# Kernel optimization log

Measured on AMD Instinct MI355X. Metric: run time of the kernel, lower is better.

Reference implementation:

```python
import jax, jax.numpy as jnp
import numpy as np

LN_EPS = 1e-5
SUM_CLAMP = 1e-12


def setup_inputs() -> dict:
    key = jax.random.key(0)
    ks = jax.random.split(key, 10)
    L, D, H, P, E = 200000, 512, 512, 16384, 200000
    lesion_x = jax.random.normal(ks[0], (L, D), dtype=jnp.float32)
    edge_index = jnp.stack([
        jax.random.randint(ks[1], (E,), 0, P),   # patient idx
        jax.random.randint(ks[2], (E,), 0, L),   # lesion idx
    ], axis=0).astype(jnp.int64)
    s1 = 1.0 / np.sqrt(D)
    s2 = 1.0 / np.sqrt(H)
    W1 = jax.random.uniform(ks[3], (H, D), jnp.float32, -s1, s1)
    b1 = jax.random.uniform(ks[4], (H,), jnp.float32, -s1, s1)
    W2 = jax.random.uniform(ks[5], (1, H), jnp.float32, -s2, s2)
    b2 = jax.random.uniform(ks[6], (1,), jnp.float32, -s2, s2)
    Wp = jax.random.uniform(ks[7], (768, D), jnp.float32, -s1, s1)
    bp = jax.random.uniform(ks[8], (768,), jnp.float32, -s1, s1)
    gamma = jnp.ones((768,), jnp.float32)
    beta = jnp.zeros((768,), jnp.float32)
    return dict(lesion_x=lesion_x, patient_to_lesion_edge_index=edge_index,
                num_patients_in_batch=P, W1=W1, b1=b1, W2=W2, b2=b2,
                Wp=Wp, bp=bp, gamma=gamma, beta=beta)


def reference(lesion_x, patient_to_lesion_edge_index, num_patients_in_batch,
              W1, b1, W2, b2, Wp, bp, gamma, beta):
    P = int(num_patients_in_batch)
    pat = patient_to_lesion_edge_index[0]
    les = patient_to_lesion_edge_index[1]
    feats = lesion_x[les]                                  # [E, D] gather
    h = jnp.tanh(feats @ W1.T + b1)                        # [E, H]
    scores = (h @ W2.T + b2)[:, 0]                         # [E]
    smax = jax.ops.segment_max(scores, pat, num_segments=P)  # [P]
    ex = jnp.exp(scores - smax[pat])                       # [E]
    esum = jax.ops.segment_sum(ex, pat, num_segments=P)
    esum = jnp.maximum(esum, SUM_CLAMP)
    alpha = ex / esum[pat]                                 # [E]
    agg = jax.ops.segment_sum(feats * alpha[:, None], pat, num_segments=P)  # [P, D]
    proj = agg @ Wp.T + bp                                 # [P, 768]
    mu = jnp.mean(proj, axis=-1, keepdims=True)
    var = jnp.mean(jnp.square(proj - mu), axis=-1, keepdims=True)
    out = (proj - mu) * jax.lax.rsqrt(var + LN_EPS) * gamma + beta
    return out
```

## Files before the change

### kernel.cpp

```cpp
#include <hip/hip_runtime.h>
#include <hip/hip_bf16.h>

#define D_DIM 512
#define H_DIM 512
#define O_DIM 768

using bf16x8 = __attribute__((ext_vector_type(8))) short;
using f32x4  = __attribute__((ext_vector_type(4))) float;

static __device__ __forceinline__ unsigned cvtpk(float lo, float hi){
  unsigned r;
  asm("v_cvt_pk_bf16_f32 %0, %1, %2" : "=v"(r) : "v"(lo), "v"(hi));
  return r;
}

static __device__ __forceinline__ float bflo(unsigned u){
  return __uint_as_float(u << 16);
}
static __device__ __forceinline__ float bfhi(unsigned u){
  return __uint_as_float(u & 0xffff0000u);
}

static __device__ __forceinline__ float fast_tanh(float x){
  float e = __expf(2.f * x);
  return 1.f - 2.f / (e + 1.f);
}

static __device__ __forceinline__ unsigned f2ord(float f){
  unsigned u = __float_as_uint(f);
  return (u & 0x80000000u) ? ~u : (u | 0x80000000u);
}
static __device__ __forceinline__ float ord2f(unsigned u){
  u = (u & 0x80000000u) ? (u & 0x7fffffffu) : ~u;
  return __uint_as_float(u);
}

static __device__ __forceinline__ void gload16(const void* g, void* l){
  __builtin_amdgcn_global_load_lds(
      (const __attribute__((address_space(1))) void*)g,
      (__attribute__((address_space(3))) void*)l, 16, 0, 0);
}

__global__ void cvt_bf16(const float* __restrict__ in,
                         unsigned short* __restrict__ out, int n8)
{
  int stride = gridDim.x * blockDim.x;
  for (int i = blockIdx.x*blockDim.x + threadIdx.x; i < n8; i += stride){
    const float4* p = (const float4*)in + (size_t)i*2;
    float4 a = p[0], b = p[1];
    uint4 pk;
    pk.x = cvtpk(a.x, a.y);
    pk.y = cvtpk(a.z, a.w);
    pk.z = cvtpk(b.x, b.y);
    pk.w = cvtpk(b.z, b.w);
    ((uint4*)out)[i] = pk;
  }
}

__launch_bounds__(256, 2)
__global__ void gemm1_db(const float* __restrict__ A,
                         const short* __restrict__ Bm,
                         const float* __restrict__ bias,
                         const float* __restrict__ w2,
                         float* __restrict__ out,
                         short* __restrict__ Ab,
                         int M, int nwg)
{
  __shared__ short lds_a[2][128*64];
  __shared__ short lds_b[2][128*64];

  const int q  = nwg >> 3, rr = nwg & 7;
  const int xcd = blockIdx.x & 7, bidx = blockIdx.x >> 3;
  const int swz = (xcd < rr ? xcd*(q+1) : rr*(q+1) + (xcd-rr)*q) + bidx;
  const int colBase = (swz & 3) * 128;
  const int rowBase = (swz >> 2) * 128;
  const bool writeAb = (colBase == 0);

  const int tid  = threadIdx.x;
  const int lane = tid & 63;
  const int w    = tid >> 6;
  const int wr   = w >> 1, wc = w & 1;
  const int lr   = lane & 15;
  const int lk   = lane >> 4;

  const int srow = tid >> 4;
  const int sgf  = tid & 15;
  const int rlocB = lane >> 3;
  const int jB    = lane & 7;

  f32x4 acc[4][4];
  #pragma unroll
  for (int i = 0; i < 4; ++i)
    #pragma unroll
    for (int j = 0; j < 4; ++j)
      acc[i][j] = (f32x4){0.f, 0.f, 0.f, 0.f};

  float4 va[8];

  #pragma unroll
  for (int c = 0; c < 8; ++c){
    int gA = rowBase + c*16 + srow; if (gA > M-1) gA = M-1;
    va[c] = *(const float4*)(A + (size_t)gA*512 + sgf*4);
  }
  #pragma unroll
  for (int c = 0; c < 4; ++c){
    int rt = w*32 + c*8 + rlocB;
    int js = jB ^ (rt & 7);
    gload16(Bm + (size_t)(colBase + rt)*512 + js*8, &lds_b[0][(w*32 + c*8)*64]);
  }
  #pragma unroll
  for (int c = 0; c < 8; ++c){
    int rt = c*16 + srow;
    uint2 pk = { cvtpk(va[c].x, va[c].y), cvtpk(va[c].z, va[c].w) };
    int sidx = (rt*64 + sgf*4) ^ ((rt & 7) << 3);
    *(uint2*)&lds_a[0][sidx] = pk;
    if (writeAb){
      int gA = rowBase + rt;
      if (gA < M) *(uint2*)(Ab + (size_t)gA*512 + sgf*4) = pk;
    }
  }
  __syncthreads();

  int cur = 0;
  for (int kt = 0; kt < 8; ++kt){
    const int nxt = cur ^ 1;
    const int kNext = (kt + 1) * 64;
    if (kt < 7){
      #pragma unroll
      for (int c = 0; c < 8; ++c){
        int gA = rowBase + c*16 + srow; if (gA > M-1) gA = M-1;
        va[c] = *(const float4*)(A + (size_t)gA*512 + kNext + sgf*4);
      }
      #pragma unroll
      for (int c = 0; c < 4; ++c){
        int rt = w*32 + c*8 + rlocB;
        int js = jB ^ (rt & 7);
        gload16(Bm + (size_t)(colBase + rt)*512 + kNext + js*8,
                &lds_b[nxt][(w*32 + c*8)*64]);
      }
    }
    #pragma unroll
    for (int kk = 0; kk < 2; ++kk){
      bf16x8 af[4], bfr[4];
      #pragma unroll
      for (int mf = 0; mf < 4; ++mf){
        int r   = wr*64 + mf*16 + lr;
        int idx = (r*64 + kk*32 + lk*8) ^ ((r & 7) << 3);
        af[mf] = *(bf16x8*)&lds_a[cur][idx];
      }
      #pragma unroll
      for (int nf = 0; nf < 4; ++nf){
        int r   = wc*64 + nf*16 + lr;
        int idx = (r*64 + kk*32 + lk*8) ^ ((r & 7) << 3);
        bfr[nf] = *(bf16x8*)&lds_b[cur][idx];
      }
      __builtin_amdgcn_s_setprio(1);
      #pragma unroll
      for (int mf = 0; mf < 4; ++mf)
        #pragma unroll
        for (int nf = 0; nf < 4; ++nf)
          acc[mf][nf] = __builtin_amdgcn_mfma_f32_16x16x32_bf16(
              af[mf], bfr[nf], acc[mf][nf], 0, 0, 0);
      __builtin_amdgcn_s_setprio(0);
    }
    if (kt < 7){
      #pragma unroll
      for (int c = 0; c < 8; ++c){
        int rt = c*16 + srow;
        uint2 pk = { cvtpk(va[c].x, va[c].y), cvtpk(va[c].z, va[c].w) };
        int sidx = (rt*64 + sgf*4) ^ ((rt & 7) << 3);
        *(uint2*)&lds_a[nxt][sidx] = pk;
        if (writeAb){
          int gA = rowBase + rt;
          if (gA < M) *(uint2*)(Ab + (size_t)gA*512 + kNext + sgf*4) = pk;
        }
      }
    }
    __syncthreads();
    cur = nxt;
  }

  #pragma unroll
  for (int mf = 0; mf < 4; ++mf){
    float part[4] = {0.f,0.f,0.f,0.f};
    #pragma unroll
    for (int nf = 0; nf < 4; ++nf){
      int gc = colBase + wc*64 + nf*16 + lr;
      float b = bias[gc], wv = w2[gc];
      #pragma unroll
      for (int r = 0; r < 4; ++r)
        part[r] += fast_tanh(acc[mf][nf][r] + b) * wv;
    }
    #pragma unroll
    for (int r = 0; r < 4; ++r){
      part[r] += __shfl_xor(part[r], 1);
      part[r] += __shfl_xor(part[r], 2);
      part[r] += __shfl_xor(part[r], 4);
      part[r] += __shfl_xor(part[r], 8);
    }
    if (lr == 0){
      int gr = rowBase + wr*64 + mf*16 + lk*4;
      #pragma unroll
      for (int r = 0; r < 4; ++r)
        if (gr + r < M) atomicAdd(&out[gr + r], part[r]);
    }
  }
}

__launch_bounds__(256, 2)
__global__ void gemm2_bf16(const short* __restrict__ A,
                           const short* __restrict__ Bm,
                           const float* __restrict__ bias,
                           float* __restrict__ out,
                           int M, int outStride)
{
  __shared__ short lds_a[128*64];
  __shared__ short lds_b[128*64];

  const int tid  = threadIdx.x;
  const int lane = tid & 63;
  const int w    = tid >> 6;
  const int wr   = w >> 1, wc = w & 1;
  const int lr   = lane & 15;
  const int lk   = lane >> 4;

  const int colBase = blockIdx.x * 128;
  const int rowBase = blockIdx.y * 128;

  f32x4 acc[4][4];
  #pragma unroll
  for (int i = 0; i < 4; ++i)
    #pragma unroll
    for (int j = 0; j < 4; ++j)
      acc[i][j] = (f32x4){0.f, 0.f, 0.f, 0.f};

  const int subrow = lane >> 3;
  const int gpre   = lane & 7;

  for (int kt = 0; kt < 512/64; ++kt){
    const int kOff = kt * 64;
    #pragma unroll
    for (int c = 0; c < 4; ++c){
      int r    = w*32 + c*8 + subrow;
      int gran = gpre ^ (r & 7);
      int gA   = rowBase + r; if (gA > M-1) gA = M-1;
      gload16(A  + (size_t)gA*512 + kOff + gran*8, &lds_a[(w*32 + c*8)*64]);
      int gB   = colBase + r;
      gload16(Bm + (size_t)gB*512 + kOff + gran*8, &lds_b[(w*32 + c*8)*64]);
    }
    __syncthreads();
    #pragma unroll
    for (int kk = 0; kk < 2; ++kk){
      bf16x8 af[4], bfr[4];
      #pragma unroll
      for (int mf = 0; mf < 4; ++mf){
        int r   = wr*64 + mf*16 + lr;
        int idx = (r*64 + kk*32 + lk*8) ^ ((r & 7) << 3);
        af[mf] = *(bf16x8*)&lds_a[idx];
      }
      #pragma unroll
      for (int nf = 0; nf < 4; ++nf){
        int r   = wc*64 + nf*16 + lr;
        int idx = (r*64 + kk*32 + lk*8) ^ ((r & 7) << 3);
        bfr[nf] = *(bf16x8*)&lds_b[idx];
      }
      #pragma unroll
      for (int mf = 0; mf < 4; ++mf)
        #pragma unroll
        for (int nf = 0; nf < 4; ++nf)
          acc[mf][nf] = __builtin_amdgcn_mfma_f32_16x16x32_bf16(
              af[mf], bfr[nf], acc[mf][nf], 0, 0, 0);
    }
    __syncthreads();
  }

  #pragma unroll
  for (int mf = 0; mf < 4; ++mf){
    int gr = rowBase + wr*64 + mf*16 + lk*4;
    #pragma unroll
    for (int nf = 0; nf < 4; ++nf){
      int gc = colBase + wc*64 + nf*16 + lr;
      float b = bias[gc];
      #pragma unroll
      for (int r = 0; r < 4; ++r)
        if (gr + r < M) out[(size_t)(gr + r)*outStride + gc] = acc[mf][nf][r] + b;
    }
  }
}

__global__ void edge_pass1(const int* __restrict__ edge, int E,
                           const float* __restrict__ scores,
                           unsigned* __restrict__ smax_o,
                           int* __restrict__ hist)
{
  int e = blockIdx.x*256 + threadIdx.x;
  if (e >= E) return;
  int p = edge[e], l = edge[E + e];
  atomicMax(&smax_o[p], f2ord(scores[l]));
  atomicAdd(&hist[p], 1);
}

__global__ void scan_kernel(const int* __restrict__ hist,
                            int* __restrict__ offsets, int P)
{
  __shared__ int s[1024];
  int t = threadIdx.x;
  int local[16]; int sum = 0;
  #pragma unroll
  for (int i = 0; i < 16; ++i){
    int idx = t*16 + i;
    local[i] = (idx < P) ? hist[idx] : 0;
    sum += local[i];
  }
  s[t] = sum;
  __syncthreads();
  for (int off = 1; off < 1024; off <<= 1){
    int v = (t >= off) ? s[t - off] : 0;
    __syncthreads();
    s[t] += v;
    __syncthreads();
  }
  int run = s[t] - sum;
  #pragma unroll
  for (int i = 0; i < 16; ++i){
    int idx = t*16 + i;
    if (idx < P) offsets[idx] = run;
    run += local[i];
  }
}

__global__ void edge_pass2(const int* __restrict__ edge, int E,
                           const float* __restrict__ scores,
                           const unsigned* __restrict__ smax_o,
                           float* __restrict__ ex,
                           float* __restrict__ esum,
                           const int* __restrict__ offsets,
                           int* __restrict__ cursor,
                           int* __restrict__ sorted)
{
  int e = blockIdx.x*256 + threadIdx.x;
  if (e >= E) return;
  int p = edge[e], l = edge[E + e];
  float v = __expf(scores[l] - ord2f(smax_o[p]));
  ex[e] = v;
  atomicAdd(&esum[p], v);
  int pos = atomicAdd(&cursor[p], 1);
  sorted[offsets[p] + pos] = e;
}

__global__ void agg_kernel(const int* __restrict__ edge, int E,
                           const short* __restrict__ Ab,
                           const float* __restrict__ ex,
                           const float* __restrict__ esum,
                           const int* __restrict__ offsets,
                           const int* __restrict__ hist,
                           const int* __restrict__ sorted,
                           unsigned* __restrict__ aggb)
{
  int p    = blockIdx.x*4 + (threadIdx.x >> 6);
  int lane = threadIdx.x & 63;
  int n = hist[p];
  if (n == 0) return;
  int start = offsets[p];
  float inv = 1.f / fmaxf(esum[p], 1e-12f);
  float a[8] = {0.f,0.f,0.f,0.f,0.f,0.f,0.f,0.f};
  int e0 = sorted[start];
  uint4 u = *(const uint4*)(Ab + (size_t)edge[E + e0]*512 + lane*8);
  float alpha = ex[e0] * inv;
  for (int i = 0; i < n; ++i){
    uint4 uc = u; float ac = alpha;
    if (i + 1 < n){
      int e2 = sorted[start + i + 1];
      u = *(const uint4*)(Ab + (size_t)edge[E + e2]*512 + lane*8);
      alpha = ex[e2] * inv;
    }
    a[0] += ac * bflo(uc.x);  a[1] += ac * bfhi(uc.x);
    a[2] += ac * bflo(uc.y);  a[3] += ac * bfhi(uc.y);
    a[4] += ac * bflo(uc.z);  a[5] += ac * bfhi(uc.z);
    a[6] += ac * bflo(uc.w);  a[7] += ac * bfhi(uc.w);
  }
  uint4 o = { cvtpk(a[0],a[1]), cvtpk(a[2],a[3]),
              cvtpk(a[4],a[5]), cvtpk(a[6],a[7]) };
  *(uint4*)&aggb[(size_t)p*256 + lane*4] = o;
}

__global__ void ln_kernel(float* __restrict__ out,
                          const float* __restrict__ gamma,
                          const float* __restrict__ beta)
{
  __shared__ float red1[4];
  __shared__ float red2[4];
  int p = blockIdx.x;
  float* row = out + (size_t)p*768;
  int t = threadIdx.x;
  float v0 = row[t], v1 = row[t+256], v2 = row[t+512];
  float s = v0 + v1 + v2;
  #pragma unroll
  for (int off = 32; off; off >>= 1) s += __shfl_down(s, off);
  int lane = t & 63, wv = t >> 6;
  if (lane == 0) red1[wv] = s;
  __syncthreads();
  float mean = (red1[0]+red1[1]+red1[2]+red1[3]) * (1.f/768.f);
  float d0 = v0-mean, d1 = v1-mean, d2 = v2-mean;
  float qq = d0*d0 + d1*d1 + d2*d2;
  #pragma unroll
  for (int off = 32; off; off >>= 1) qq += __shfl_down(qq, off);
  if (lane == 0) red2[wv] = qq;
  __syncthreads();
  float var = (red2[0]+red2[1]+red2[2]+red2[3]) * (1.f/768.f);
  float inv = rsqrtf(var + 1e-5f);
  row[t]     = d0*inv*gamma[t]     + beta[t];
  row[t+256] = d1*inv*gamma[t+256] + beta[t+256];
  row[t+512] = d2*inv*gamma[t+512] + beta[t+512];
}

extern "C" void kernel_launch(void* const* d_in, const int* in_sizes, int n_in,
                              void* d_out, int out_size, void* d_ws, size_t ws_size,
                              hipStream_t stream)
{
  const float* lesion_x = (const float*)d_in[0];
  const int*   edge     = (const int*)d_in[1];
  const float* W1    = (const float*)d_in[3];
  const float* b1    = (const float*)d_in[4];
  const float* W2    = (const float*)d_in[5];
  const float* Wp    = (const float*)d_in[7];
  const float* bp    = (const float*)d_in[8];
  const float* gamma = (const float*)d_in[9];
  const float* beta  = (const float*)d_in[10];

  const int L = in_sizes[0] / D_DIM;
  const int E = in_sizes[1] / 2;
  const int P = out_size / O_DIM;

  auto al = [](size_t x){ return (x + 255) & ~(size_t)255; };
  char* ws = (char*)d_ws;
  size_t oScores = 0;
  size_t oSmax   = oScores + al((size_t)L*4);
  size_t oEsum   = oSmax   + al((size_t)P*4);
  size_t oHist   = oEsum   + al((size_t)P*4);
  size_t oCursor = oHist   + al((size_t)P*4);
  size_t smallEnd= oCursor + al((size_t)P*4);
  size_t oAggB   = smallEnd;
  size_t aggEnd  = oAggB   + al((size_t)P*D_DIM*2);
  size_t oOff    = aggEnd;
  size_t oEx     = oOff    + al((size_t)P*4);
  size_t oSorted = oEx     + al((size_t)E*4);
  size_t oW1b    = oSorted + al((size_t)E*4);
  size_t oWpb    = oW1b    + al((size_t)H_DIM*D_DIM*2);
  size_t oAb     = oWpb    + al((size_t)O_DIM*D_DIM*2);
  size_t need    = oAb     + al((size_t)L*D_DIM*2);
  (void)need;

  float*    scores = (float*)(ws + oScores);
  unsigned* smax_o = (unsigned*)(ws + oSmax);
  float*    esum   = (float*)(ws + oEsum);
  int*      hist   = (int*)(ws + oHist);
  int*      cursor = (int*)(ws + oCursor);
  unsigned* aggb   = (unsigned*)(ws + oAggB);
  int*      offs   = (int*)(ws + oOff);
  float*    ex     = (float*)(ws + oEx);
  int*      sorted = (int*)(ws + oSorted);
  short*    W1b    = (short*)(ws + oW1b);
  short*    Wpb    = (short*)(ws + oWpb);
  short*    Ab     = (short*)(ws + oAb);

  hipMemsetAsync(d_ws, 0, smallEnd, stream);
  hipMemsetAsync(ws + oAggB, 0, (size_t)P*D_DIM*2, stream);

  dim3 b256(256);
  int eb = (E + 255) / 256;

  cvt_bf16<<<128, b256, 0, stream>>>(W1, (unsigned short*)W1b, H_DIM*D_DIM/8);
  cvt_bf16<<<192, b256, 0, stream>>>(Wp, (unsigned short*)Wpb, O_DIM*D_DIM/8);

  int nRow = (L + 127) / 128;
  int nwg  = 4 * nRow;
  gemm1_db<<<nwg, b256, 0, stream>>>(lesion_x, W1b, b1, W2, scores, Ab, L, nwg);

  edge_pass1<<<eb, b256, 0, stream>>>(edge, E, scores, smax_o, hist);
  scan_kernel<<<1, 1024, 0, stream>>>(hist, offs, P);
  edge_pass2<<<eb, b256, 0, stream>>>(edge, E, scores, smax_o, ex, esum,
                                      offs, cursor, sorted);
  agg_kernel<<<P/4, b256, 0, stream>>>(edge, E, Ab, ex, esum, offs,
                                       hist, sorted, aggb);
  gemm2_bf16<<<dim3(O_DIM/128, P/128), b256, 0, stream>>>(
      (const short*)aggb, Wpb, bp, (float*)d_out, P, O_DIM);
  ln_kernel<<<P, b256, 0, stream>>>((float*)d_out, gamma, beta);
}
```

Before: 469.9 us.

## Fuse LayerNorm into projection GEMM and single-buffer A tile in gemm1

The projection GEMM becomes a 512-thread kernel where each block computes 64 full rows of 768 outputs, then does the LayerNorm reduction in registers and LDS before writing the final output, removing the separate LN kernel and its read-modify-write of the output. Variance is computed as E[x^2]-mu^2, which is less numerically robust than the two-pass form. Separately, gemm1 drops the double-buffered A tile in LDS and adds an extra barrier so it can target 3 blocks per CU instead of 2, trading an extra sync per k-step for occupancy.

```diff
diff --git a/kernel.cpp b/kernel.cpp
--- a/kernel.cpp
+++ b/kernel.cpp
@@ -57,8 +57,8 @@
   }
 }
 
-__launch_bounds__(256, 2)
-__global__ void gemm1_db(const float* __restrict__ A,
+__launch_bounds__(256, 3)
+__global__ void gemm1_p2(const float* __restrict__ A,
                          const short* __restrict__ Bm,
                          const float* __restrict__ bias,
                          const float* __restrict__ w2,
@@ -66,7 +66,7 @@
                          short* __restrict__ Ab,
                          int M, int nwg)
 {
-  __shared__ short lds_a[2][128*64];
+  __shared__ short lds_a[128*64];
   __shared__ short lds_b[2][128*64];
 
   const int q  = nwg >> 3, rr = nwg & 7;
@@ -113,7 +113,7 @@
     int rt = c*16 + srow;
     uint2 pk = { cvtpk(va[c].x, va[c].y), cvtpk(va[c].z, va[c].w) };
     int sidx = (rt*64 + sgf*4) ^ ((rt & 7) << 3);
-    *(uint2*)&lds_a[0][sidx] = pk;
+    *(uint2*)&lds_a[sidx] = pk;
     if (writeAb){
       int gA = rowBase + rt;
       if (gA < M) *(uint2*)(Ab + (size_t)gA*512 + sgf*4) = pk;
@@ -124,18 +124,18 @@
   int cur = 0;
   for (int kt = 0; kt < 8; ++kt){
     const int nxt = cur ^ 1;
-    const int kNext = (kt + 1) * 64;
+    const int kN = (kt + 1) * 64;
     if (kt < 7){
       #pragma unroll
       for (int c = 0; c < 8; ++c){
         int gA = rowBase + c*16 + srow; if (gA > M-1) gA = M-1;
-        va[c] = *(const float4*)(A + (size_t)gA*512 + kNext + sgf*4);
+        va[c] = *(const float4*)(A + (size_t)gA*512 + kN + sgf*4);
       }
       #pragma unroll
       for (int c = 0; c < 4; ++c){
         int rt = w*32 + c*8 + rlocB;
         int js = jB ^ (rt & 7);
-        gload16(Bm + (size_t)(colBase + rt)*512 + kNext + js*8,
+        gload16(Bm + (size_t)(colBase + rt)*512 + kN + js*8,
                 &lds_b[nxt][(w*32 + c*8)*64]);
       }
     }
@@ -146,7 +146,7 @@
       for (int mf = 0; mf < 4; ++mf){
         int r   = wr*64 + mf*16 + lr;
         int idx = (r*64 + kk*32 + lk*8) ^ ((r & 7) << 3);
-        af[mf] = *(bf16x8*)&lds_a[cur][idx];
+        af[mf] = *(bf16x8*)&lds_a[idx];
       }
       #pragma unroll
       for (int nf = 0; nf < 4; ++nf){
@@ -163,20 +163,21 @@
               af[mf], bfr[nf], acc[mf][nf], 0, 0, 0);
       __builtin_amdgcn_s_setprio(0);
     }
+    __syncthreads();
     if (kt < 7){
       #pragma unroll
       for (int c = 0; c < 8; ++c){
         int rt = c*16 + srow;
         uint2 pk = { cvtpk(va[c].x, va[c].y), cvtpk(va[c].z, va[c].w) };
         int sidx = (rt*64 + sgf*4) ^ ((rt & 7) << 3);
-        *(uint2*)&lds_a[nxt][sidx] = pk;
+        *(uint2*)&lds_a[sidx] = pk;
         if (writeAb){
           int gA = rowBase + rt;
-          if (gA < M) *(uint2*)(Ab + (size_t)gA*512 + kNext + sgf*4) = pk;
+          if (gA < M) *(uint2*)(Ab + (size_t)gA*512 + kN + sgf*4) = pk;
         }
       }
-    }
-    __syncthreads();
+      __syncthreads();
+    }
     cur = nxt;
   }
 
@@ -207,85 +208,142 @@
   }
 }
 
-__launch_bounds__(256, 2)
-__global__ void gemm2_bf16(const short* __restrict__ A,
-                           const short* __restrict__ Bm,
-                           const float* __restrict__ bias,
-                           float* __restrict__ out,
-                           int M, int outStride)
-{
-  __shared__ short lds_a[128*64];
-  __shared__ short lds_b[128*64];
+__launch_bounds__(512, 1)
+__global__ void gemm2_ln(const short* __restrict__ A,
+                         const short* __restrict__ Bm,
+                         const float* __restrict__ bp,
+                         const float* __restrict__ gamma,
+                         const float* __restrict__ beta,
+                         float* __restrict__ out)
+{
+  __shared__ short lds_a[64*64];
+  __shared__ short lds_b[768*64];
+  __shared__ float redS[64*8];
+  __shared__ float redQ[64*8];
+  __shared__ float muArr[64];
+  __shared__ float invArr[64];
 
   const int tid  = threadIdx.x;
   const int lane = tid & 63;
   const int w    = tid >> 6;
-  const int wr   = w >> 1, wc = w & 1;
   const int lr   = lane & 15;
   const int lk   = lane >> 4;
-
-  const int colBase = blockIdx.x * 128;
-  const int rowBase = blockIdx.y * 128;
-
-  f32x4 acc[4][4];
+  const int rowBase = blockIdx.x * 64;
+  const int rloc = lane >> 3;
+  const int jg   = lane & 7;
+
+  f32x4 acc[4][6];
   #pragma unroll
   for (int i = 0; i < 4; ++i)
     #pragma unroll
-    for (int j = 0; j < 4; ++j)
+    for (int j = 0; j < 6; ++j)
       acc[i][j] = (f32x4){0.f, 0.f, 0.f, 0.f};
 
-  const int subrow = lane >> 3;
-  const int gpre   = lane & 7;
-
-  for (int kt = 0; kt < 512/64; ++kt){
+  for (int kt = 0; kt < 8; ++kt){
     const int kOff = kt * 64;
-    #pragma unroll
-    for (int c = 0; c < 4; ++c){
-      int r    = w*32 + c*8 + subrow;
-      int gran = gpre ^ (r & 7);
-      int gA   = rowBase + r; if (gA > M-1) gA = M-1;
-      gload16(A  + (size_t)gA*512 + kOff + gran*8, &lds_a[(w*32 + c*8)*64]);
-      int gB   = colBase + r;
-      gload16(Bm + (size_t)gB*512 + kOff + gran*8, &lds_b[(w*32 + c*8)*64]);
+    {
+      int rt = w*8 + rloc;
+      int js = jg ^ (rt & 7);
+      gload16(A + (size_t)(rowBase + rt)*512 + kOff + js*8, &lds_a[(w*8)*64]);
+    }
+    #pragma unroll
+    for (int c = 0; c < 12; ++c){
+      int rt = w*96 + c*8 + rloc;
+      int js = jg ^ (rt & 7);
+      gload16(Bm + (size_t)rt*512 + kOff + js*8, &lds_b[(w*96 + c*8)*64]);
     }
     __syncthreads();
     #pragma unroll
     for (int kk = 0; kk < 2; ++kk){
-      bf16x8 af[4], bfr[4];
+      bf16x8 af[4], bfr[6];
       #pragma unroll
       for (int mf = 0; mf < 4; ++mf){
-        int r   = wr*64 + mf*16 + lr;
+        int r   = mf*16 + lr;
         int idx = (r*64 + kk*32 + lk*8) ^ ((r & 7) << 3);
         af[mf] = *(bf16x8*)&lds_a[idx];
       }
       #pragma unroll
-      for (int nf = 0; nf < 4; ++nf){
-        int r   = wc*64 + nf*16 + lr;
+      for (int nf = 0; nf < 6; ++nf){
+        int r   = w*96 + nf*16 + lr;
         int idx = (r*64 + kk*32 + lk*8) ^ ((r & 7) << 3);
         bfr[nf] = *(bf16x8*)&lds_b[idx];
       }
+      __builtin_amdgcn_s_setprio(1);
       #pragma unroll
       for (int mf = 0; mf < 4; ++mf)
         #pragma unroll
-        for (int nf = 0; nf < 4; ++nf)
+        for (int nf = 0; nf < 6; ++nf)
           acc[mf][nf] = __builtin_amdgcn_mfma_f32_16x16x32_bf16(
               af[mf], bfr[nf], acc[mf][nf], 0, 0, 0);
+      __builtin_amdgcn_s_setprio(0);
     }
     __syncthreads();
   }
 
-  #pragma unroll
-  for (int mf = 0; mf < 4; ++mf){
-    int gr = rowBase + wr*64 + mf*16 + lk*4;
-    #pragma unroll
-    for (int nf = 0; nf < 4; ++nf){
-      int gc = colBase + wc*64 + nf*16 + lr;
-      float b = bias[gc];
-      #pragma unroll
-      for (int r = 0; r < 4; ++r)
-        if (gr + r < M) out[(size_t)(gr + r)*outStride + gc] = acc[mf][nf][r] + b;
-    }
-  }
+  float s1[4][4], s2[4][4];
+  #pragma unroll
+  for (int mf = 0; mf < 4; ++mf)
+    #pragma unroll
+    for (int r = 0; r < 4; ++r){ s1[mf][r] = 0.f; s2[mf][r] = 0.f; }
+  #pragma unroll
+  for (int mf = 0; mf < 4; ++mf)
+    #pragma unroll
+    for (int nf = 0; nf < 6; ++nf){
+      int gc = w*96 + nf*16 + lr;
+      float b = bp[gc];
+      #pragma unroll
+      for (int r = 0; r < 4; ++r){
+        float v = acc[mf][nf][r] + b;
+        s1[mf][r] += v;
+        s2[mf][r] += v*v;
+      }
+    }
+  #pragma unroll
+  for (int mf = 0; mf < 4; ++mf)
+    #pragma unroll
+    for (int r = 0; r < 4; ++r){
+      #pragma unroll
+      for (int d = 1; d < 16; d <<= 1){
+        s1[mf][r] += __shfl_xor(s1[mf][r], d);
+        s2[mf][r] += __shfl_xor(s2[mf][r], d);
+      }
+    }
+  if (lr == 0){
+    #pragma unroll
+    for (int mf = 0; mf < 4; ++mf)
+      #pragma unroll
+      for (int r = 0; r < 4; ++r){
+        int row = mf*16 + lk*4 + r;
+        redS[row*8 + w] = s1[mf][r];
+        redQ[row*8 + w] = s2[mf][r];
+      }
+  }
+  __syncthreads();
+  if (tid < 64){
+    float s = 0.f, qq = 0.f;
+    #pragma unroll
+    for (int j = 0; j < 8; ++j){ s += redS[tid*8 + j]; qq += redQ[tid*8 + j]; }
+    float mu  = s * (1.f/768.f);
+    float var = qq * (1.f/768.f) - mu*mu;
+    muArr[tid]  = mu;
+    invArr[tid] = rsqrtf(var + 1e-5f);
+  }
+  __syncthreads();
+
+  #pragma unroll
+  for (int mf = 0; mf < 4; ++mf)
+    #pragma unroll
+    for (int nf = 0; nf < 6; ++nf){
+      int gc = w*96 + nf*16 + lr;
+      float b = bp[gc], g = gamma[gc], be = beta[gc];
+      #pragma unroll
+      for (int r = 0; r < 4; ++r){
+        int row = mf*16 + lk*4 + r;
+        float v = acc[mf][nf][r] + b;
+        out[(size_t)(rowBase + row)*768 + gc] =
+            (v - muArr[row]) * invArr[row] * g + be;
+      }
+    }
 }
 
 __global__ void edge_pass1(const int* __restrict__ edge, int E,
@@ -382,36 +440,6 @@
   uint4 o = { cvtpk(a[0],a[1]), cvtpk(a[2],a[3]),
               cvtpk(a[4],a[5]), cvtpk(a[6],a[7]) };
   *(uint4*)&aggb[(size_t)p*256 + lane*4] = o;
-}
-
-__global__ void ln_kernel(float* __restrict__ out,
-                          const float* __restrict__ gamma,
-                          const float* __restrict__ beta)
-{
-  __shared__ float red1[4];
-  __shared__ float red2[4];
-  int p = blockIdx.x;
-  float* row = out + (size_t)p*768;
-  int t = threadIdx.x;
-  float v0 = row[t], v1 = row[t+256], v2 = row[t+512];
-  float s = v0 + v1 + v2;
-  #pragma unroll
-  for (int off = 32; off; off >>= 1) s += __shfl_down(s, off);
-  int lane = t & 63, wv = t >> 6;
-  if (lane == 0) red1[wv] = s;
-  __syncthreads();
-  float mean = (red1[0]+red1[1]+red1[2]+red1[3]) * (1.f/768.f);
-  float d0 = v0-mean, d1 = v1-mean, d2 = v2-mean;
-  float qq = d0*d0 + d1*d1 + d2*d2;
-  #pragma unroll
-  for (int off = 32; off; off >>= 1) qq += __shfl_down(qq, off);
-  if (lane == 0) red2[wv] = qq;
-  __syncthreads();
-  float var = (red2[0]+red2[1]+red2[2]+red2[3]) * (1.f/768.f);
-  float inv = rsqrtf(var + 1e-5f);
-  row[t]     = d0*inv*gamma[t]     + beta[t];
-  row[t+256] = d1*inv*gamma[t+256] + beta[t+256];
-  row[t+512] = d2*inv*gamma[t+512] + beta[t+512];
 }
 
 extern "C" void kernel_launch(void* const* d_in, const int* in_sizes, int n_in,
@@ -475,7 +503,7 @@
 
   int nRow = (L + 127) / 128;
   int nwg  = 4 * nRow;
-  gemm1_db<<<nwg, b256, 0, stream>>>(lesion_x, W1b, b1, W2, scores, Ab, L, nwg);
+  gemm1_p2<<<nwg, b256, 0, stream>>>(lesion_x, W1b, b1, W2, scores, Ab, L, nwg);
 
   edge_pass1<<<eb, b256, 0, stream>>>(edge, E, scores, smax_o, hist);
   scan_kernel<<<1, 1024, 0, stream>>>(hist, offs, P);
@@ -483,7 +511,6 @@
                                       offs, cursor, sorted);
   agg_kernel<<<P/4, b256, 0, stream>>>(edge, E, Ab, ex, esum, offs,
                                        hist, sorted, aggb);
-  gemm2_bf16<<<dim3(O_DIM/128, P/128), b256, 0, stream>>>(
-      (const short*)aggb, Wpb, bp, (float*)d_out, P, O_DIM);
-  ln_kernel<<<P, b256, 0, stream>>>((float*)d_out, gamma, beta);
-}
+  gemm2_ln<<<P/64, dim3(512), 0, stream>>>((const short*)aggb, Wpb, bp,
+                                           gamma, beta, (float*)d_out);
+}
```

New measurement: 669.5 us. 42.5% more time.
